# Performance work log

Hardware: AMD Instinct MI355X
Metric: run time of the kernel (lower is better)

The kernel has to match this reference:

```python
import jax, jax.numpy as jnp
import numpy as np

EPS = 1e-10

def setup_inputs() -> dict:
    key = jax.random.key(0)
    ks = jax.random.split(key, 7)
    B, S, C, H, W = 8, 4, 512, 64, 64
    Cq = C // 4
    x = jax.random.normal(ks[0], (B, S, C, H, W), dtype=jnp.float32)
    wq = jax.random.normal(ks[1], (S, Cq, C), dtype=jnp.float32) * 0.02
    bq = jax.random.normal(ks[2], (S, Cq), dtype=jnp.float32) * 0.02
    wk = jax.random.normal(ks[3], (S, Cq, C), dtype=jnp.float32) * 0.02
    bk = jax.random.normal(ks[4], (S, Cq), dtype=jnp.float32) * 0.02
    wv = jax.random.normal(ks[5], (S, C, C), dtype=jnp.float32) * 0.02
    bv = jax.random.normal(ks[6], (S, C), dtype=jnp.float32) * 0.02
    gamma = jnp.zeros((1,), dtype=jnp.float32)
    return {"x": x, "wq": wq, "bq": bq, "wk": wk, "bk": bk,
            "wv": wv, "bv": bv, "gamma": gamma}

def reference(x, wq, bq, wk, bk, wv, bv, gamma):
    # x: (B, S, C, H, W); per-scale 1x1 convs == per-pixel matmuls
    B, S, C, H, W = x.shape
    q = jnp.einsum('bschw,soc->bsohw', x, wq) + bq[None, :, :, None, None]
    k = jnp.einsum('bschw,soc->bsohw', x, wk) + bk[None, :, :, None, None]
    v = jnp.einsum('bschw,soc->bsohw', x, wv) + bv[None, :, :, None, None]
    pq = q.reshape(B, S, -1)                      # (B, S, D)
    pk = k.reshape(B, S, -1).transpose(0, 2, 1)   # (B, D, S)
    pv = v.reshape(B, S, -1)                      # (B, S, C*H*W)
    # L2 normalization (cosine similarity), matching torch eps placement
    A1 = pq / (jnp.sqrt(jnp.sum(pq * pq, axis=-1, keepdims=True)) + EPS)
    B1 = pk / (jnp.sqrt(jnp.sum(pk * pk, axis=1, keepdims=True)) + EPS)
    energy = jnp.einsum('bsd,bdt->bst', A1, B1)   # (B, S, S)
    attention = jax.nn.softmax(energy, axis=-1)
    out = jnp.einsum('bst,btd->bsd', attention, pv).reshape(B, S, C, H, W)
    out = gamma[0] * out + x
    # original returns list [out[:, i]] for i in range(S); return stacked tensor
    return out
```

## Files before the change

kernel.cpp:

```cpp
#include <hip/hip_runtime.h>
#include <hip/hip_bf16.h>

#define EPS_F 1e-10f

typedef short s16x8 __attribute__((ext_vector_type(8)));
typedef float f32x4 __attribute__((ext_vector_type(4)));
typedef unsigned short ushort_t;

constexpr int B_ = 8, S_ = 4, C_ = 512, Cq_ = 128, HW_ = 4096;
constexpr long long D_ = (long long)Cq_ * HW_;

__device__ inline float bf_lo(unsigned int u) { return __uint_as_float(u << 16); }
__device__ inline float bf_hi(unsigned int u) { return __uint_as_float(u & 0xffff0000u); }

__device__ inline ushort_t f2bf(float f) {
    __hip_bfloat16 h = __float2bfloat16(f);
    return *reinterpret_cast<ushort_t*>(&h);
}
__device__ inline unsigned int pack_bf2(float a, float b) {
    return (unsigned int)f2bf(a) | ((unsigned int)f2bf(b) << 16);
}

#define GLOAD16(gp, lp) __builtin_amdgcn_global_load_lds( \
    (const __attribute__((address_space(1))) unsigned int*)(gp), \
    (__attribute__((address_space(3))) unsigned int*)(lp), 16, 0, 0)

__global__ __launch_bounds__(256) void prep3(
    const float* __restrict__ wq, const float* __restrict__ wk,
    const float* __restrict__ wv,
    ushort_t* __restrict__ Wqk_pre, ushort_t* __restrict__ Wvb_pre,
    float* __restrict__ g4) {
    int gid = blockIdx.x * 256 + threadIdx.x;
    if (gid < 32 * 6 * 4) g4[gid] = 0.f;
    if (gid < 65536) {
        int s = gid >> 14;
        int kt = (gid >> 11) & 7;
        int row = (gid >> 3) & 255;
        int slot = gid & 7;
        int col = kt * 64 + ((slot ^ (row & 7)) << 3);
        const float* src = (row < 128)
            ? &wq[((size_t)s * 128 + row) * 512 + col]
            : &wk[((size_t)s * 128 + (row - 128)) * 512 + col];
        float4 f0 = *reinterpret_cast<const float4*>(src);
        float4 f1 = *reinterpret_cast<const float4*>(src + 4);
        uint4 o;
        o.x = pack_bf2(f0.x, f0.y); o.y = pack_bf2(f0.z, f0.w);
        o.z = pack_bf2(f1.x, f1.y); o.w = pack_bf2(f1.z, f1.w);
        *reinterpret_cast<uint4*>(Wqk_pre + (size_t)gid * 8) = o;
    } else {
        int c2 = gid - 65536;
        int t = c2 >> 15;
        int ct = (c2 >> 14) & 1;
        int kt = (c2 >> 11) & 7;
        int row = (c2 >> 3) & 255;
        int slot = c2 & 7;
        int col = kt * 64 + ((slot ^ (row & 7)) << 3);
        const float* src = &wv[((size_t)t * 512 + ct * 256 + row) * 512 + col];
        float4 f0 = *reinterpret_cast<const float4*>(src);
        float4 f1 = *reinterpret_cast<const float4*>(src + 4);
        uint4 o;
        o.x = pack_bf2(f0.x, f0.y); o.y = pack_bf2(f0.z, f0.w);
        o.z = pack_bf2(f1.x, f1.y); o.w = pack_bf2(f1.z, f1.w);
        *reinterpret_cast<uint4*>(Wvb_pre + (size_t)c2 * 8) = o;
    }
}

#define STAGE_A(tilebase, buf, Asarr)                                        \
    {                                                                        \
        const ushort_t* _tp = (tilebase);                                    \
        _Pragma("unroll")                                                    \
        for (int _i = 0; _i < 4; ++_i)                                       \
            GLOAD16(_tp + ((w4 + _i) << 9) + (lane << 3),                    \
                    &Asarr[buf][(w4 + _i) << 9]);                            \
    }

#define COMPUTE_STEP(buf, Asarr, Bsarr, accv)                                \
    {                                                                        \
        _Pragma("unroll")                                                    \
        for (int h = 0; h < 2; ++h) {                                        \
            s16x8 af0, af1, af2, af3, bf0, bf1;                              \
            af0 = *reinterpret_cast<const s16x8*>(                           \
                &Asarr[buf][(arow + 0 * 16 + li) * 64 + a_sl[h]]);           \
            af1 = *reinterpret_cast<const s16x8*>(                           \
                &Asarr[buf][(arow + 1 * 16 + li) * 64 + a_sl[h]]);           \
            af2 = *reinterpret_cast<const s16x8*>(                           \
                &Asarr[buf][(arow + 2 * 16 + li) * 64 + a_sl[h]]);           \
            af3 = *reinterpret_cast<const s16x8*>(                           \
                &Asarr[buf][(arow + 3 * 16 + li) * 64 + a_sl[h]]);           \
            bf0 = *reinterpret_cast<const s16x8*>(                           \
                &Bsarr[buf][bp0 * 64 + b_sl0[h]]);                           \
            bf1 = *reinterpret_cast<const s16x8*>(                           \
                &Bsarr[buf][bp1 * 64 + b_sl1[h]]);                           \
            accv[0][0] = __builtin_amdgcn_mfma_f32_16x16x32_bf16(af0, bf0, accv[0][0], 0, 0, 0); \
            accv[0][1] = __builtin_amdgcn_mfma_f32_16x16x32_bf16(af0, bf1, accv[0][1], 0, 0, 0); \
            accv[1][0] = __builtin_amdgcn_mfma_f32_16x16x32_bf16(af1, bf0, accv[1][0], 0, 0, 0); \
            accv[1][1] = __builtin_amdgcn_mfma_f32_16x16x32_bf16(af1, bf1, accv[1][1], 0, 0, 0); \
            accv[2][0] = __builtin_amdgcn_mfma_f32_16x16x32_bf16(af2, bf0, accv[2][0], 0, 0, 0); \
            accv[2][1] = __builtin_amdgcn_mfma_f32_16x16x32_bf16(af2, bf1, accv[2][1], 0, 0, 0); \
            accv[3][0] = __builtin_amdgcn_mfma_f32_16x16x32_bf16(af3, bf0, accv[3][0], 0, 0, 0); \
            accv[3][1] = __builtin_amdgcn_mfma_f32_16x16x32_bf16(af3, bf1, accv[3][1], 0, 0, 0); \
        }                                                                    \
    }

#define WRITE_B(buf, Bsarr, v0, v1)                                          \
    {                                                                        \
        float _vv[8] = {v0.x, v0.y, v0.z, v0.w, v1.x, v1.y, v1.z, v1.w};     \
        ushort_t* _d = &Bsarr[buf][bwbase];                                  \
        _Pragma("unroll")                                                    \
        for (int _j = 0; _j < 8; ++_j) _d[_j * 64] = f2bf(_vv[_j]);          \
    }

__global__ __launch_bounds__(512) void qk3(
    const ushort_t* __restrict__ Wqk_pre, const float* __restrict__ x,
    const float* __restrict__ bq, const float* __restrict__ bk,
    ushort_t* __restrict__ Qb, ushort_t* __restrict__ Kb) {

    const int bt = blockIdx.z;
    const int s = bt & 3;
    const int p0 = blockIdx.x * 64;

    __shared__ __align__(16) ushort_t As[2][16384];
    __shared__ __align__(16) ushort_t Bs[2][4096];

    const int tid = threadIdx.x;
    const int w = tid >> 6, lane = tid & 63;
    const int w4 = w * 4;
    const int wr = w >> 1, wc = w & 1;
    const int li = lane & 15, lk = lane >> 4;
    const int arow = wr * 64;
    int a_sl[2], b_sl0[2], b_sl1[2];
    const int bp0 = wc * 32 + 0 * 16 + li, bp1 = wc * 32 + 1 * 16 + li;
#pragma unroll
    for (int h = 0; h < 2; ++h) {
        a_sl[h] = (((h * 4 + lk) ^ (li & 7)) << 3);
        b_sl0[h] = (((h * 4 + lk) ^ ((bp0 >> 3) & 7)) << 3);
        b_sl1[h] = (((h * 4 + lk) ^ ((bp1 >> 3) & 7)) << 3);
    }
    const int sk = tid >> 3, sp = (tid & 7) * 8;
    const int bwbase = sp * 64 + (((sk >> 3) ^ (tid & 7)) << 3) + (sk & 7);

    const float* Bx = x + (size_t)bt * C_ * HW_ + p0 + sp;

    f32x4 acc[4][2];
#pragma unroll
    for (int mf = 0; mf < 4; ++mf)
#pragma unroll
        for (int nf = 0; nf < 2; ++nf) acc[mf][nf] = 0.f;

    STAGE_A(Wqk_pre + (((size_t)s * 8 + 0) << 14), 0, As);
    {
        const float* src = Bx + (size_t)sk * HW_;
        float4 v0 = *reinterpret_cast<const float4*>(src);
        float4 v1 = *reinterpret_cast<const float4*>(src + 4);
        WRITE_B(0, Bs, v0, v1);
    }
    __syncthreads();

    int cur = 0;
    for (int st = 0; st < 8; ++st) {
        float4 nb0, nb1;
        const bool more = (st < 7);
        if (more) {
            STAGE_A(Wqk_pre + (((size_t)s * 8 + st + 1) << 14), cur ^ 1, As);
            const float* src = Bx + (size_t)((st + 1) * 64 + sk) * HW_;
            nb0 = *reinterpret_cast<const float4*>(src);
            nb1 = *reinterpret_cast<const float4*>(src + 4);
        }
        COMPUTE_STEP(cur, As, Bs, acc);
        if (more) {
            WRITE_B(cur ^ 1, Bs, nb0, nb1);
            __syncthreads();
            cur ^= 1;
        }
    }

#pragma unroll
    for (int mf = 0; mf < 4; ++mf) {
#pragma unroll
        for (int r = 0; r < 4; ++r) {
            int m = wr * 64 + mf * 16 + lk * 4 + r;
            float bias = (m < 128) ? bq[s * 128 + m] : bk[s * 128 + (m - 128)];
#pragma unroll
            for (int nf = 0; nf < 2; ++nf) {
                int p = p0 + wc * 32 + nf * 16 + li;
                float vv = acc[mf][nf][r] + bias;
                if (m < 128)
                    Qb[(size_t)bt * D_ + (size_t)m * HW_ + p] = f2bf(vv);
                else
                    Kb[(size_t)bt * D_ + (size_t)(m - 128) * HW_ + p] = f2bf(vv);
            }
        }
    }
}

__global__ __launch_bounds__(256) void gram_part(
    const ushort_t* __restrict__ Q, const ushort_t* __restrict__ K,
    float* __restrict__ g4) {

    const int u = blockIdx.x, ch = blockIdx.y, bs = blockIdx.z;
    const int b = bs >> 2;
    const ushort_t *pa, *pb;
    if (u < 4)       { pa = Q + (size_t)bs * D_; pb = K + (size_t)(b * 4 + u) * D_; }
    else if (u == 4) { pa = pb = Q + (size_t)bs * D_; }
    else             { pa = pb = K + (size_t)bs * D_; }

    const size_t off = (size_t)ch * (D_ / 4);
    const uint4* va = reinterpret_cast<const uint4*>(pa + off);
    const uint4* vb = reinterpret_cast<const uint4*>(pb + off);
    const int n8 = (int)(D_ / 4 / 8);

    float acc = 0.f;
    for (int i = threadIdx.x; i < n8; i += 256) {
        uint4 a = va[i], c = vb[i];
        acc += bf_lo(a.x) * bf_lo(c.x) + bf_hi(a.x) * bf_hi(c.x);
        acc += bf_lo(a.y) * bf_lo(c.y) + bf_hi(a.y) * bf_hi(c.y);
        acc += bf_lo(a.z) * bf_lo(c.z) + bf_hi(a.z) * bf_hi(c.z);
        acc += bf_lo(a.w) * bf_lo(c.w) + bf_hi(a.w) * bf_hi(c.w);
    }
#pragma unroll
    for (int o = 32; o > 0; o >>= 1) acc += __shfl_down(acc, o);

    __shared__ float wsum[4];
    const int lane = threadIdx.x & 63, wid = threadIdx.x >> 6;
    if (lane == 0) wsum[wid] = acc;
    __syncthreads();
    if (threadIdx.x == 0)
        g4[(size_t)(bs * 6 + u) * 4 + ch] = wsum[0] + wsum[1] + wsum[2] + wsum[3];
}

__global__ void att_k(const float* __restrict__ g4, float* __restrict__ att) {
    const int b = threadIdx.x;
    if (b >= B_) return;
    auto g = [&](int s, int u) {
        const float* p = g4 + (size_t)((b * 4 + s) * 6 + u) * 4;
        return p[0] + p[1] + p[2] + p[3];
    };
    float nq[4], nk[4];
#pragma unroll
    for (int s = 0; s < 4; ++s) {
        nq[s] = sqrtf(g(s, 4)) + EPS_F;
        nk[s] = sqrtf(g(s, 5)) + EPS_F;
    }
#pragma unroll
    for (int s = 0; s < 4; ++s) {
        float e[4], m = -1e30f;
#pragma unroll
        for (int t = 0; t < 4; ++t) {
            e[t] = g(s, t) / (nq[s] * nk[t]);
            m = fmaxf(m, e[t]);
        }
        float sum = 0.f;
#pragma unroll
        for (int t = 0; t < 4; ++t) { e[t] = expf(e[t] - m); sum += e[t]; }
#pragma unroll
        for (int t = 0; t < 4; ++t) att[(size_t)(b * 4 + s) * 4 + t] = e[t] / sum;
    }
}

__global__ __launch_bounds__(512) void vblend3(
    const ushort_t* __restrict__ Wvb_pre, const float* __restrict__ x,
    const float* __restrict__ bv, const float* __restrict__ att,
    const float* __restrict__ gamma, float* __restrict__ out) {

    const int b = blockIdx.z;
    const int ct = blockIdx.y;
    const int p0 = blockIdx.x * 64;

    __shared__ __align__(16) ushort_t As[2][16384];
    __shared__ __align__(16) ushort_t Bs[2][4096];

    const int tid = threadIdx.x;
    const int w = tid >> 6, lane = tid & 63;
    const int w4 = w * 4;
    const int wr = w >> 1, wc = w & 1;
    const int li = lane & 15, lk = lane >> 4;
    const int arow = wr * 64;
    int a_sl[2], b_sl0[2], b_sl1[2];
    const int bp0 = wc * 32 + 0 * 16 + li, bp1 = wc * 32 + 1 * 16 + li;
#pragma unroll
    for (int h = 0; h < 2; ++h) {
        a_sl[h] = (((h * 4 + lk) ^ (li & 7)) << 3);
        b_sl0[h] = (((h * 4 + lk) ^ ((bp0 >> 3) & 7)) << 3);
        b_sl1[h] = (((h * 4 + lk) ^ ((bp1 >> 3) & 7)) << 3);
    }
    const int sk = tid >> 3, sp = (tid & 7) * 8;
    const int bwbase = sp * 64 + (((sk >> 3) ^ (tid & 7)) << 3) + (sk & 7);
    const float gm = gamma[0];

    f32x4 mst[4][4][2];
#pragma unroll
    for (int so = 0; so < 4; ++so)
#pragma unroll
        for (int mf = 0; mf < 4; ++mf)
#pragma unroll
            for (int nf = 0; nf < 2; ++nf) mst[so][mf][nf] = 0.f;

    f32x4 acc[4][2];
#pragma unroll
    for (int mf = 0; mf < 4; ++mf)
#pragma unroll
        for (int nf = 0; nf < 2; ++nf) acc[mf][nf] = 0.f;

    STAGE_A(Wvb_pre + (((size_t)(0 * 2 + ct) * 8 + 0) << 14), 0, As);
    {
        const float* src = x + ((size_t)(b * 4 + 0) * 512 + sk) * HW_ + p0 + sp;
        float4 v0 = *reinterpret_cast<const float4*>(src);
        float4 v1 = *reinterpret_cast<const float4*>(src + 4);
        WRITE_B(0, Bs, v0, v1);
    }
    __syncthreads();

    int cur = 0;
    for (int st = 0; st < 32; ++st) {
        float4 nb0, nb1;
        const bool more = (st < 31);
        if (more) {
            const int t2 = (st + 1) >> 3, kt2 = (st + 1) & 7;
            STAGE_A(Wvb_pre + (((size_t)(t2 * 2 + ct) * 8 + kt2) << 14), cur ^ 1, As);
            const float* src =
                x + ((size_t)(b * 4 + t2) * 512 + kt2 * 64 + sk) * HW_ + p0 + sp;
            nb0 = *reinterpret_cast<const float4*>(src);
            nb1 = *reinterpret_cast<const float4*>(src + 4);
        }
        COMPUTE_STEP(cur, As, Bs, acc);
        if ((st & 7) == 7) {
            const int t = st >> 3;
#pragma unroll
            for (int so = 0; so < 4; ++so) {
                const float wt = att[(size_t)(b * 4 + so) * 4 + t];
#pragma unroll
                for (int mf = 0; mf < 4; ++mf)
#pragma unroll
                    for (int nf = 0; nf < 2; ++nf)
                        mst[so][mf][nf] += wt * acc[mf][nf];
            }
#pragma unroll
            for (int mf = 0; mf < 4; ++mf)
#pragma unroll
                for (int nf = 0; nf < 2; ++nf) acc[mf][nf] = 0.f;
        }
        if (more) {
            WRITE_B(cur ^ 1, Bs, nb0, nb1);
            __syncthreads();
            cur ^= 1;
        }
    }

    const int c0 = ct * 256;
#pragma unroll
    for (int mf = 0; mf < 4; ++mf) {
#pragma unroll
        for (int r = 0; r < 4; ++r) {
            int c = c0 + wr * 64 + mf * 16 + lk * 4 + r;
            float bvv[4];
#pragma unroll
            for (int t = 0; t < 4; ++t) bvv[t] = bv[(size_t)t * 512 + c];
#pragma unroll
            for (int so = 0; so < 4; ++so) {
                float a0 = att[(size_t)(b * 4 + so) * 4 + 0];
                float a1 = att[(size_t)(b * 4 + so) * 4 + 1];
                float a2 = att[(size_t)(b * 4 + so) * 4 + 2];
                float a3 = att[(size_t)(b * 4 + so) * 4 + 3];
                float bsum = a0 * bvv[0] + a1 * bvv[1] + a2 * bvv[2] + a3 * bvv[3];
#pragma unroll
                for (int nf = 0; nf < 2; ++nf) {
                    int p = p0 + wc * 32 + nf * 16 + li;
                    size_t off = ((size_t)(b * 4 + so) * C_ + c) * HW_ + p;
                    out[off] = gm * (mst[so][mf][nf][r] + bsum) + x[off];
                }
            }
        }
    }
}

extern "C" void kernel_launch(void* const* d_in, const int* in_sizes, int n_in,
                              void* d_out, int out_size, void* d_ws, size_t ws_size,
                              hipStream_t stream) {
    const float* x     = (const float*)d_in[0];
    const float* wq    = (const float*)d_in[1];
    const float* bq    = (const float*)d_in[2];
    const float* wk    = (const float*)d_in[3];
    const float* bk    = (const float*)d_in[4];
    const float* wv    = (const float*)d_in[5];
    const float* bv    = (const float*)d_in[6];
    const float* gamma = (const float*)d_in[7];
    float* out = (float*)d_out;

    char* ws = (char*)d_ws;
    const size_t qk_elems = (size_t)B_ * S_ * Cq_ * HW_;
    ushort_t* Qb      = (ushort_t*)ws;
    ushort_t* Kb      = Qb + qk_elems;
    ushort_t* Wqk_pre = Kb + qk_elems;
    ushort_t* Wvb_pre = Wqk_pre + (size_t)4 * 8 * 256 * 64;
    float*    g4      = (float*)(Wvb_pre + (size_t)4 * 2 * 8 * 256 * 64);
    float*    att     = g4 + 32 * 6 * 4;

    prep3<<<768, 256, 0, stream>>>(wq, wk, wv, Wqk_pre, Wvb_pre, g4);
    qk3<<<dim3(64, 1, 32), 512, 0, stream>>>(Wqk_pre, x, bq, bk, Qb, Kb);
    gram_part<<<dim3(6, 4, 32), 256, 0, stream>>>(Qb, Kb, g4);
    att_k<<<1, 64, 0, stream>>>(g4, att);
    vblend3<<<dim3(64, 2, 8), 512, 0, stream>>>(Wvb_pre, x, bv, att, gamma, out);
}
```

Baseline: 414.0 us.

## Triple-buffer GEMM pipelines, remap blocks, and fuse gram reductions per batch

The QK and V-blend GEMM kernels move from a double-buffered loop with __syncthreads to a shared triple-buffered pipeline. It uses explicit vmcnt/lgkmcnt waits, raw s_barrier, MFMA priority boosting, and a new XOR swizzle for B-tile writes. Blocks are launched on a 1D grid with an id remap that interleaves the ordering, likely for L2/XCD locality. The gram kernel now reads each Q/K chunk once and accumulates all 24 dot products per batch instead of launching separate blocks per pair, and attention weights are cached in LDS. The larger LDS footprint from triple buffering may reduce occupancy.

```diff
diff --git a/kernel.cpp b/kernel.cpp
--- a/kernel.cpp
+++ b/kernel.cpp
@@ -20,10 +20,20 @@
 __device__ inline unsigned int pack_bf2(float a, float b) {
     return (unsigned int)f2bf(a) | ((unsigned int)f2bf(b) << 16);
 }
+__device__ inline float dot8(uint4 a, uint4 b) {
+    return bf_lo(a.x) * bf_lo(b.x) + bf_hi(a.x) * bf_hi(b.x)
+         + bf_lo(a.y) * bf_lo(b.y) + bf_hi(a.y) * bf_hi(b.y)
+         + bf_lo(a.z) * bf_lo(b.z) + bf_hi(a.z) * bf_hi(b.z)
+         + bf_lo(a.w) * bf_lo(b.w) + bf_hi(a.w) * bf_hi(b.w);
+}
 
 #define GLOAD16(gp, lp) __builtin_amdgcn_global_load_lds( \
     (const __attribute__((address_space(1))) unsigned int*)(gp), \
     (__attribute__((address_space(3))) unsigned int*)(lp), 16, 0, 0)
+
+#define VMCNT(n) asm volatile("s_waitcnt vmcnt(" #n ")" ::: "memory")
+#define LGK0     asm volatile("s_waitcnt lgkmcnt(0)" ::: "memory")
+#define MFMA16(a, b, c) __builtin_amdgcn_mfma_f32_16x16x32_bf16(a, b, c, 0, 0, 0)
 
 __global__ __launch_bounds__(256) void prep3(
     const float* __restrict__ wq, const float* __restrict__ wk,
@@ -31,7 +41,7 @@
     ushort_t* __restrict__ Wqk_pre, ushort_t* __restrict__ Wvb_pre,
     float* __restrict__ g4) {
     int gid = blockIdx.x * 256 + threadIdx.x;
-    if (gid < 32 * 6 * 4) g4[gid] = 0.f;
+    if (gid < 8 * 24 * 16) g4[gid] = 0.f;
     if (gid < 65536) {
         int s = gid >> 14;
         int kt = (gid >> 11) & 7;
@@ -65,113 +75,130 @@
     }
 }
 
-#define STAGE_A(tilebase, buf, Asarr)                                        \
+#define STAGE_A(T, bufidx)                                                   \
+    { const ushort_t* _tp = ASRC(T);                                         \
+      ushort_t* _ld = &AsAll[(bufidx) * 16384];                              \
+      _Pragma("unroll")                                                      \
+      for (int _i = 0; _i < 4; ++_i)                                         \
+          GLOAD16(_tp + ((w4 + _i) << 9) + (lane << 3),                      \
+                  _ld + ((w4 + _i) << 9)); }
+
+#define LOAD_B(T, V0, V1)                                                    \
+    { const float* _s = BSRC(T);                                             \
+      V0 = *reinterpret_cast<const float4*>(_s);                             \
+      V1 = *reinterpret_cast<const float4*>(_s + 4); }
+
+#define WRITE_B(bufidx, V0, V1)                                              \
+    { float _vv[8] = {V0.x, V0.y, V0.z, V0.w, V1.x, V1.y, V1.z, V1.w};       \
+      ushort_t* _bd = &BsAll[(bufidx) * 4096 + bw_row0];                     \
+      _Pragma("unroll")                                                      \
+      for (int _j = 0; _j < 8; ++_j)                                         \
+          _bd[_j * 64 + ((bw_sb ^ _j) << 3)] = f2bf(_vv[_j]); }
+
+#define COMPUTE(bufidx)                                                      \
+    { const int _ab = (bufidx) * 16384, _bb = (bufidx) * 4096;               \
+      _Pragma("unroll")                                                      \
+      for (int h = 0; h < 2; ++h) {                                          \
+          s16x8 af0 = *reinterpret_cast<const s16x8*>(                       \
+              &AsAll[_ab + (arow + 0 * 16 + li) * 64 + a_sl[h]]);            \
+          s16x8 af1 = *reinterpret_cast<const s16x8*>(                       \
+              &AsAll[_ab + (arow + 1 * 16 + li) * 64 + a_sl[h]]);            \
+          s16x8 af2 = *reinterpret_cast<const s16x8*>(                       \
+              &AsAll[_ab + (arow + 2 * 16 + li) * 64 + a_sl[h]]);            \
+          s16x8 af3 = *reinterpret_cast<const s16x8*>(                       \
+              &AsAll[_ab + (arow + 3 * 16 + li) * 64 + a_sl[h]]);            \
+          s16x8 bf0 = *reinterpret_cast<const s16x8*>(                       \
+              &BsAll[_bb + bp0 * 64 + b_sl0[h]]);                            \
+          s16x8 bf1 = *reinterpret_cast<const s16x8*>(                       \
+              &BsAll[_bb + bp1 * 64 + b_sl1[h]]);                            \
+          __builtin_amdgcn_s_setprio(1);                                     \
+          acc[0][0] = MFMA16(af0, bf0, acc[0][0]);                           \
+          acc[0][1] = MFMA16(af0, bf1, acc[0][1]);                           \
+          acc[1][0] = MFMA16(af1, bf0, acc[1][0]);                           \
+          acc[1][1] = MFMA16(af1, bf1, acc[1][1]);                           \
+          acc[2][0] = MFMA16(af2, bf0, acc[2][0]);                           \
+          acc[2][1] = MFMA16(af2, bf1, acc[2][1]);                           \
+          acc[3][0] = MFMA16(af3, bf0, acc[3][0]);                           \
+          acc[3][1] = MFMA16(af3, bf1, acc[3][1]);                           \
+          __builtin_amdgcn_s_setprio(0);                                     \
+      } }
+
+#define PIPE_PROLOGUE()                                                      \
+    LOAD_B(0, nbE0, nbE1);                                                   \
+    STAGE_A(0, 0);                                                           \
+    LOAD_B(1, nbO0, nbO1);                                                   \
+    STAGE_A(1, 1);                                                           \
+    VMCNT(10);                                                               \
+    WRITE_B(0, nbE0, nbE1);                                                  \
+    VMCNT(6);                                                                \
+    LGK0;                                                                    \
+    __builtin_amdgcn_s_barrier();
+
+#define PIPE_ITER(T, WB0, WB1, LB0, LB1)                                     \
     {                                                                        \
-        const ushort_t* _tp = (tilebase);                                    \
+        const int _t = (T);                                                  \
+        if (_t + 1 < NT) { VMCNT(4); WRITE_B(oN, WB0, WB1); }                \
+        if (_t + 2 < NT) { LOAD_B(_t + 2, LB0, LB1); STAGE_A(_t + 2, oNN); } \
+        COMPUTE(oC);                                                         \
+        ITER_EXTRA(_t);                                                      \
+        if (_t + 1 < NT) {                                                   \
+            if (_t + 2 < NT) { VMCNT(6); } else { VMCNT(0); }                \
+            LGK0;                                                            \
+            __builtin_amdgcn_s_barrier();                                    \
+        }                                                                    \
+        int _r = oC; oC = oN; oN = oNN; oNN = _r;                            \
+    }
+
+#define PIPE_COMMON_DECLS()                                                  \
+    const int tid = threadIdx.x;                                             \
+    const int w = tid >> 6, lane = tid & 63;                                 \
+    const int w4 = w * 4;                                                    \
+    const int wr = w >> 1, wc = w & 1;                                       \
+    const int li = lane & 15, lk = lane >> 4;                                \
+    const int arow = wr * 64;                                                \
+    const int bp0 = wc * 32 + li, bp1 = wc * 32 + 16 + li;                   \
+    int a_sl[2], b_sl0[2], b_sl1[2];                                         \
+    _Pragma("unroll")                                                        \
+    for (int h = 0; h < 2; ++h) {                                            \
+        a_sl[h] = (((h * 4 + lk) ^ (li & 7)) << 3);                          \
+        b_sl0[h] = (((h * 4 + lk) ^ ((bp0 >> 3) & 7) ^ (bp0 & 7)) << 3);     \
+        b_sl1[h] = (((h * 4 + lk) ^ ((bp1 >> 3) & 7) ^ (bp1 & 7)) << 3);     \
+    }                                                                        \
+    const int sk = tid >> 3, sp = (tid & 7) * 8;                             \
+    const int bw_row0 = sp * 64 + ((tid >> 3) & 7);                          \
+    const int bw_sb = (tid >> 6) ^ (tid & 7);                                \
+    int oC = 0, oN = 1, oNN = 2;                                             \
+    float4 nbE0, nbE1, nbO0, nbO1;                                           \
+    f32x4 acc[4][2];                                                         \
+    _Pragma("unroll")                                                        \
+    for (int mf = 0; mf < 4; ++mf)                                           \
         _Pragma("unroll")                                                    \
-        for (int _i = 0; _i < 4; ++_i)                                       \
-            GLOAD16(_tp + ((w4 + _i) << 9) + (lane << 3),                    \
-                    &Asarr[buf][(w4 + _i) << 9]);                            \
-    }
-
-#define COMPUTE_STEP(buf, Asarr, Bsarr, accv)                                \
-    {                                                                        \
-        _Pragma("unroll")                                                    \
-        for (int h = 0; h < 2; ++h) {                                        \
-            s16x8 af0, af1, af2, af3, bf0, bf1;                              \
-            af0 = *reinterpret_cast<const s16x8*>(                           \
-                &Asarr[buf][(arow + 0 * 16 + li) * 64 + a_sl[h]]);           \
-            af1 = *reinterpret_cast<const s16x8*>(                           \
-                &Asarr[buf][(arow + 1 * 16 + li) * 64 + a_sl[h]]);           \
-            af2 = *reinterpret_cast<const s16x8*>(                           \
-                &Asarr[buf][(arow + 2 * 16 + li) * 64 + a_sl[h]]);           \
-            af3 = *reinterpret_cast<const s16x8*>(                           \
-                &Asarr[buf][(arow + 3 * 16 + li) * 64 + a_sl[h]]);           \
-            bf0 = *reinterpret_cast<const s16x8*>(                           \
-                &Bsarr[buf][bp0 * 64 + b_sl0[h]]);                           \
-            bf1 = *reinterpret_cast<const s16x8*>(                           \
-                &Bsarr[buf][bp1 * 64 + b_sl1[h]]);                           \
-            accv[0][0] = __builtin_amdgcn_mfma_f32_16x16x32_bf16(af0, bf0, accv[0][0], 0, 0, 0); \
-            accv[0][1] = __builtin_amdgcn_mfma_f32_16x16x32_bf16(af0, bf1, accv[0][1], 0, 0, 0); \
-            accv[1][0] = __builtin_amdgcn_mfma_f32_16x16x32_bf16(af1, bf0, accv[1][0], 0, 0, 0); \
-            accv[1][1] = __builtin_amdgcn_mfma_f32_16x16x32_bf16(af1, bf1, accv[1][1], 0, 0, 0); \
-            accv[2][0] = __builtin_amdgcn_mfma_f32_16x16x32_bf16(af2, bf0, accv[2][0], 0, 0, 0); \
-            accv[2][1] = __builtin_amdgcn_mfma_f32_16x16x32_bf16(af2, bf1, accv[2][1], 0, 0, 0); \
-            accv[3][0] = __builtin_amdgcn_mfma_f32_16x16x32_bf16(af3, bf0, accv[3][0], 0, 0, 0); \
-            accv[3][1] = __builtin_amdgcn_mfma_f32_16x16x32_bf16(af3, bf1, accv[3][1], 0, 0, 0); \
-        }                                                                    \
-    }
-
-#define WRITE_B(buf, Bsarr, v0, v1)                                          \
-    {                                                                        \
-        float _vv[8] = {v0.x, v0.y, v0.z, v0.w, v1.x, v1.y, v1.z, v1.w};     \
-        ushort_t* _d = &Bsarr[buf][bwbase];                                  \
-        _Pragma("unroll")                                                    \
-        for (int _j = 0; _j < 8; ++_j) _d[_j * 64] = f2bf(_vv[_j]);          \
-    }
-
-__global__ __launch_bounds__(512) void qk3(
+        for (int nf = 0; nf < 2; ++nf) acc[mf][nf] = 0.f;
+
+#define ASRC(T) (Wqk_pre + ((size_t)(s * 8 + (T)) << 14))
+#define BSRC(T) (x + (size_t)bt * C_ * HW_ + (size_t)((T) * 64 + sk) * HW_ + p0 + sp)
+#define ITER_EXTRA(T)
+
+__global__ __launch_bounds__(512) void qk4(
     const ushort_t* __restrict__ Wqk_pre, const float* __restrict__ x,
     const float* __restrict__ bq, const float* __restrict__ bk,
     ushort_t* __restrict__ Qb, ushort_t* __restrict__ Kb) {
 
-    const int bt = blockIdx.z;
+    constexpr int NT = 8;
+    const int id = ((blockIdx.x & 7) << 8) | (blockIdx.x >> 3);
+    const int bt = id >> 6;
     const int s = bt & 3;
-    const int p0 = blockIdx.x * 64;
-
-    __shared__ __align__(16) ushort_t As[2][16384];
-    __shared__ __align__(16) ushort_t Bs[2][4096];
-
-    const int tid = threadIdx.x;
-    const int w = tid >> 6, lane = tid & 63;
-    const int w4 = w * 4;
-    const int wr = w >> 1, wc = w & 1;
-    const int li = lane & 15, lk = lane >> 4;
-    const int arow = wr * 64;
-    int a_sl[2], b_sl0[2], b_sl1[2];
-    const int bp0 = wc * 32 + 0 * 16 + li, bp1 = wc * 32 + 1 * 16 + li;
-#pragma unroll
-    for (int h = 0; h < 2; ++h) {
-        a_sl[h] = (((h * 4 + lk) ^ (li & 7)) << 3);
-        b_sl0[h] = (((h * 4 + lk) ^ ((bp0 >> 3) & 7)) << 3);
-        b_sl1[h] = (((h * 4 + lk) ^ ((bp1 >> 3) & 7)) << 3);
-    }
-    const int sk = tid >> 3, sp = (tid & 7) * 8;
-    const int bwbase = sp * 64 + (((sk >> 3) ^ (tid & 7)) << 3) + (sk & 7);
-
-    const float* Bx = x + (size_t)bt * C_ * HW_ + p0 + sp;
-
-    f32x4 acc[4][2];
-#pragma unroll
-    for (int mf = 0; mf < 4; ++mf)
-#pragma unroll
-        for (int nf = 0; nf < 2; ++nf) acc[mf][nf] = 0.f;
-
-    STAGE_A(Wqk_pre + (((size_t)s * 8 + 0) << 14), 0, As);
-    {
-        const float* src = Bx + (size_t)sk * HW_;
-        float4 v0 = *reinterpret_cast<const float4*>(src);
-        float4 v1 = *reinterpret_cast<const float4*>(src + 4);
-        WRITE_B(0, Bs, v0, v1);
-    }
-    __syncthreads();
-
-    int cur = 0;
-    for (int st = 0; st < 8; ++st) {
-        float4 nb0, nb1;
-        const bool more = (st < 7);
-        if (more) {
-            STAGE_A(Wqk_pre + (((size_t)s * 8 + st + 1) << 14), cur ^ 1, As);
-            const float* src = Bx + (size_t)((st + 1) * 64 + sk) * HW_;
-            nb0 = *reinterpret_cast<const float4*>(src);
-            nb1 = *reinterpret_cast<const float4*>(src + 4);
-        }
-        COMPUTE_STEP(cur, As, Bs, acc);
-        if (more) {
-            WRITE_B(cur ^ 1, Bs, nb0, nb1);
-            __syncthreads();
-            cur ^= 1;
-        }
+    const int p0 = (id & 63) * 64;
+
+    __shared__ __align__(16) ushort_t AsAll[3 * 16384];
+    __shared__ __align__(16) ushort_t BsAll[3 * 4096];
+
+    PIPE_COMMON_DECLS();
+    PIPE_PROLOGUE();
+
+    for (int t0 = 0; t0 < NT; t0 += 2) {
+        PIPE_ITER(t0,     nbO0, nbO1, nbE0, nbE1);
+        PIPE_ITER(t0 + 1, nbE0, nbE1, nbO0, nbO1);
     }
 
 #pragma unroll
@@ -192,160 +219,67 @@
         }
     }
 }
-
-__global__ __launch_bounds__(256) void gram_part(
-    const ushort_t* __restrict__ Q, const ushort_t* __restrict__ K,
-    float* __restrict__ g4) {
-
-    const int u = blockIdx.x, ch = blockIdx.y, bs = blockIdx.z;
-    const int b = bs >> 2;
-    const ushort_t *pa, *pb;
-    if (u < 4)       { pa = Q + (size_t)bs * D_; pb = K + (size_t)(b * 4 + u) * D_; }
-    else if (u == 4) { pa = pb = Q + (size_t)bs * D_; }
-    else             { pa = pb = K + (size_t)bs * D_; }
-
-    const size_t off = (size_t)ch * (D_ / 4);
-    const uint4* va = reinterpret_cast<const uint4*>(pa + off);
-    const uint4* vb = reinterpret_cast<const uint4*>(pb + off);
-    const int n8 = (int)(D_ / 4 / 8);
-
-    float acc = 0.f;
-    for (int i = threadIdx.x; i < n8; i += 256) {
-        uint4 a = va[i], c = vb[i];
-        acc += bf_lo(a.x) * bf_lo(c.x) + bf_hi(a.x) * bf_hi(c.x);
-        acc += bf_lo(a.y) * bf_lo(c.y) + bf_hi(a.y) * bf_hi(c.y);
-        acc += bf_lo(a.z) * bf_lo(c.z) + bf_hi(a.z) * bf_hi(c.z);
-        acc += bf_lo(a.w) * bf_lo(c.w) + bf_hi(a.w) * bf_hi(c.w);
-    }
-#pragma unroll
-    for (int o = 32; o > 0; o >>= 1) acc += __shfl_down(acc, o);
-
-    __shared__ float wsum[4];
-    const int lane = threadIdx.x & 63, wid = threadIdx.x >> 6;
-    if (lane == 0) wsum[wid] = acc;
-    __syncthreads();
-    if (threadIdx.x == 0)
-        g4[(size_t)(bs * 6 + u) * 4 + ch] = wsum[0] + wsum[1] + wsum[2] + wsum[3];
-}
-
-__global__ void att_k(const float* __restrict__ g4, float* __restrict__ att) {
-    const int b = threadIdx.x;
-    if (b >= B_) return;
-    auto g = [&](int s, int u) {
-        const float* p = g4 + (size_t)((b * 4 + s) * 6 + u) * 4;
-        return p[0] + p[1] + p[2] + p[3];
-    };
-    float nq[4], nk[4];
-#pragma unroll
-    for (int s = 0; s < 4; ++s) {
-        nq[s] = sqrtf(g(s, 4)) + EPS_F;
-        nk[s] = sqrtf(g(s, 5)) + EPS_F;
-    }
-#pragma unroll
-    for (int s = 0; s < 4; ++s) {
-        float e[4], m = -1e30f;
-#pragma unroll
-        for (int t = 0; t < 4; ++t) {
-            e[t] = g(s, t) / (nq[s] * nk[t]);
-            m = fmaxf(m, e[t]);
-        }
-        float sum = 0.f;
-#pragma unroll
-        for (int t = 0; t < 4; ++t) { e[t] = expf(e[t] - m); sum += e[t]; }
-#pragma unroll
-        for (int t = 0; t < 4; ++t) att[(size_t)(b * 4 + s) * 4 + t] = e[t] / sum;
-    }
-}
-
-__global__ __launch_bounds__(512) void vblend3(
+#undef ASRC
+#undef BSRC
+#undef ITER_EXTRA
+
+#define ASRC(T) (Wvb_pre + (((size_t)(((T) >> 3) * 2 + ct) * 8 + ((T) & 7)) << 14))
+#define BSRC(T) (x + ((size_t)(b * 4 + ((T) >> 3)) * 512 + ((T) & 7) * 64 + sk) * HW_ + p0 + sp)
+#define ITER_EXTRA(T)                                                        \
+    if (((T) & 7) == 7) {                                                    \
+        const int _t2 = (T) >> 3;                                            \
+        float _wv[4];                                                        \
+        _Pragma("unroll")                                                    \
+        for (int _so = 0; _so < 4; ++_so) _wv[_so] = attL[_so * 4 + _t2];    \
+        _Pragma("unroll")                                                    \
+        for (int _so = 0; _so < 4; ++_so)                                    \
+            _Pragma("unroll")                                                \
+            for (int _mf = 0; _mf < 4; ++_mf)                                \
+                _Pragma("unroll")                                            \
+                for (int _nf = 0; _nf < 2; ++_nf)                            \
+                    mst[_so][_mf][_nf] += _wv[_so] * acc[_mf][_nf];          \
+        _Pragma("unroll")                                                    \
+        for (int _mf = 0; _mf < 4; ++_mf)                                    \
+            _Pragma("unroll")                                                \
+            for (int _nf = 0; _nf < 2; ++_nf) acc[_mf][_nf] = 0.f;           \
+    }
+
+__global__ __launch_bounds__(512) void vblend4(
     const ushort_t* __restrict__ Wvb_pre, const float* __restrict__ x,
     const float* __restrict__ bv, const float* __restrict__ att,
     const float* __restrict__ gamma, float* __restrict__ out) {
 
-    const int b = blockIdx.z;
-    const int ct = blockIdx.y;
-    const int p0 = blockIdx.x * 64;
-
-    __shared__ __align__(16) ushort_t As[2][16384];
-    __shared__ __align__(16) ushort_t Bs[2][4096];
-
-    const int tid = threadIdx.x;
-    const int w = tid >> 6, lane = tid & 63;
-    const int w4 = w * 4;
-    const int wr = w >> 1, wc = w & 1;
-    const int li = lane & 15, lk = lane >> 4;
-    const int arow = wr * 64;
-    int a_sl[2], b_sl0[2], b_sl1[2];
-    const int bp0 = wc * 32 + 0 * 16 + li, bp1 = wc * 32 + 1 * 16 + li;
-#pragma unroll
-    for (int h = 0; h < 2; ++h) {
-        a_sl[h] = (((h * 4 + lk) ^ (li & 7)) << 3);
-        b_sl0[h] = (((h * 4 + lk) ^ ((bp0 >> 3) & 7)) << 3);
-        b_sl1[h] = (((h * 4 + lk) ^ ((bp1 >> 3) & 7)) << 3);
-    }
-    const int sk = tid >> 3, sp = (tid & 7) * 8;
-    const int bwbase = sp * 64 + (((sk >> 3) ^ (tid & 7)) << 3) + (sk & 7);
+    constexpr int NT = 32;
+    const int id = ((blockIdx.x & 7) << 7) | (blockIdx.x >> 3);
+    const int b = id >> 7;
+    const int ct = (id >> 6) & 1;
+    const int p0 = (id & 63) * 64;
+
+    __shared__ __align__(16) ushort_t AsAll[3 * 16384];
+    __shared__ __align__(16) ushort_t BsAll[3 * 4096];
+    __shared__ float attL[16];
+
+    if (threadIdx.x < 16) attL[threadIdx.x] = att[b * 16 + threadIdx.x];
+    __syncthreads();
+
+    PIPE_COMMON_DECLS();
+
+    f32x4 mst[4][4][2];
+#pragma unroll
+    for (int so = 0; so < 4; ++so)
+#pragma unroll
+        for (int mf = 0; mf < 4; ++mf)
+#pragma unroll
+            for (int nf = 0; nf < 2; ++nf) mst[so][mf][nf] = 0.f;
+
+    PIPE_PROLOGUE();
+
+    for (int t0 = 0; t0 < NT; t0 += 2) {
+        PIPE_ITER(t0,     nbO0, nbO1, nbE0, nbE1);
+        PIPE_ITER(t0 + 1, nbE0, nbE1, nbO0, nbO1);
+    }
+
     const float gm = gamma[0];
-
-    f32x4 mst[4][4][2];
-#pragma unroll
-    for (int so = 0; so < 4; ++so)
-#pragma unroll
-        for (int mf = 0; mf < 4; ++mf)
-#pragma unroll
-            for (int nf = 0; nf < 2; ++nf) mst[so][mf][nf] = 0.f;
-
-    f32x4 acc[4][2];
-#pragma unroll
-    for (int mf = 0; mf < 4; ++mf)
-#pragma unroll
-        for (int nf = 0; nf < 2; ++nf) acc[mf][nf] = 0.f;
-
-    STAGE_A(Wvb_pre + (((size_t)(0 * 2 + ct) * 8 + 0) << 14), 0, As);
-    {
-        const float* src = x + ((size_t)(b * 4 + 0) * 512 + sk) * HW_ + p0 + sp;
-        float4 v0 = *reinterpret_cast<const float4*>(src);
-        float4 v1 = *reinterpret_cast<const float4*>(src + 4);
-        WRITE_B(0, Bs, v0, v1);
-    }
-    __syncthreads();
-
-    int cur = 0;
-    for (int st = 0; st < 32; ++st) {
-        float4 nb0, nb1;
-        const bool more = (st < 31);
-        if (more) {
-            const int t2 = (st + 1) >> 3, kt2 = (st + 1) & 7;
-            STAGE_A(Wvb_pre + (((size_t)(t2 * 2 + ct) * 8 + kt2) << 14), cur ^ 1, As);
-            const float* src =
-                x + ((size_t)(b * 4 + t2) * 512 + kt2 * 64 + sk) * HW_ + p0 + sp;
-            nb0 = *reinterpret_cast<const float4*>(src);
-            nb1 = *reinterpret_cast<const float4*>(src + 4);
-        }
-        COMPUTE_STEP(cur, As, Bs, acc);
-        if ((st & 7) == 7) {
-            const int t = st >> 3;
-#pragma unroll
-            for (int so = 0; so < 4; ++so) {
-                const float wt = att[(size_t)(b * 4 + so) * 4 + t];
-#pragma unroll
-                for (int mf = 0; mf < 4; ++mf)
-#pragma unroll
-                    for (int nf = 0; nf < 2; ++nf)
-                        mst[so][mf][nf] += wt * acc[mf][nf];
-            }
-#pragma unroll
-            for (int mf = 0; mf < 4; ++mf)
-#pragma unroll
-                for (int nf = 0; nf < 2; ++nf) acc[mf][nf] = 0.f;
-        }
-        if (more) {
-            WRITE_B(cur ^ 1, Bs, nb0, nb1);
-            __syncthreads();
-            cur ^= 1;
-        }
-    }
-
     const int c0 = ct * 256;
 #pragma unroll
     for (int mf = 0; mf < 4; ++mf) {
@@ -357,11 +291,8 @@
             for (int t = 0; t < 4; ++t) bvv[t] = bv[(size_t)t * 512 + c];
 #pragma unroll
             for (int so = 0; so < 4; ++so) {
-                float a0 = att[(size_t)(b * 4 + so) * 4 + 0];
-                float a1 = att[(size_t)(b * 4 + so) * 4 + 1];
-                float a2 = att[(size_t)(b * 4 + so) * 4 + 2];
-                float a3 = att[(size_t)(b * 4 + so) * 4 + 3];
-                float bsum = a0 * bvv[0] + a1 * bvv[1] + a2 * bvv[2] + a3 * bvv[3];
+                float bsum = attL[so * 4 + 0] * bvv[0] + attL[so * 4 + 1] * bvv[1]
+                           + attL[so * 4 + 2] * bvv[2] + attL[so * 4 + 3] * bvv[3];
 #pragma unroll
                 for (int nf = 0; nf < 2; ++nf) {
                     int p = p0 + wc * 32 + nf * 16 + li;
@@ -370,6 +301,94 @@
                 }
             }
         }
+    }
+}
+#undef ASRC
+#undef BSRC
+#undef ITER_EXTRA
+
+__global__ __launch_bounds__(256) void gram5(
+    const ushort_t* __restrict__ Q, const ushort_t* __restrict__ K,
+    float* __restrict__ g4) {
+
+    const int ch = blockIdx.x;
+    const int b  = blockIdx.y;
+    const size_t base = (size_t)ch * (D_ / 16);
+
+    const uint4* qv[4];
+    const uint4* kv[4];
+#pragma unroll
+    for (int s = 0; s < 4; ++s) {
+        qv[s] = reinterpret_cast<const uint4*>(Q + (size_t)(b * 4 + s) * D_ + base);
+        kv[s] = reinterpret_cast<const uint4*>(K + (size_t)(b * 4 + s) * D_ + base);
+    }
+
+    float accr[24];
+#pragma unroll
+    for (int e = 0; e < 24; ++e) accr[e] = 0.f;
+
+    const int n8 = (int)(D_ / 16 / 8);
+    for (int i = threadIdx.x; i < n8; i += 256) {
+        uint4 qa[4], ka[4];
+#pragma unroll
+        for (int s = 0; s < 4; ++s) { qa[s] = qv[s][i]; ka[s] = kv[s][i]; }
+#pragma unroll
+        for (int s = 0; s < 4; ++s) {
+#pragma unroll
+            for (int u = 0; u < 4; ++u) accr[s * 4 + u] += dot8(qa[s], ka[u]);
+            accr[16 + s] += dot8(qa[s], qa[s]);
+            accr[20 + s] += dot8(ka[s], ka[s]);
+        }
+    }
+
+    __shared__ float red[4][24];
+    const int lane = threadIdx.x & 63, wid = threadIdx.x >> 6;
+#pragma unroll
+    for (int e = 0; e < 24; ++e) {
+        float v = accr[e];
+#pragma unroll
+        for (int o = 32; o > 0; o >>= 1) v += __shfl_down(v, o);
+        if (lane == 0) red[wid][e] = v;
+    }
+    __syncthreads();
+    if (threadIdx.x < 24) {
+        float t = red[0][threadIdx.x] + red[1][threadIdx.x]
+                + red[2][threadIdx.x] + red[3][threadIdx.x];
+        g4[((size_t)b * 24 + threadIdx.x) * 16 + ch] = t;
+    }
+}
+
+__global__ void att_k5(const float* __restrict__ g4, float* __restrict__ att) {
+    const int b = threadIdx.x;
+    if (b >= B_) return;
+    float e_[24];
+#pragma unroll
+    for (int e = 0; e < 24; ++e) {
+        const float* p = g4 + ((size_t)b * 24 + e) * 16;
+        float t = 0.f;
+#pragma unroll
+        for (int ch = 0; ch < 16; ++ch) t += p[ch];
+        e_[e] = t;
+    }
+    float nq[4], nk[4];
+#pragma unroll
+    for (int s = 0; s < 4; ++s) {
+        nq[s] = sqrtf(e_[16 + s]) + EPS_F;
+        nk[s] = sqrtf(e_[20 + s]) + EPS_F;
+    }
+#pragma unroll
+    for (int s = 0; s < 4; ++s) {
+        float e[4], m = -1e30f;
+#pragma unroll
+        for (int t = 0; t < 4; ++t) {
+            e[t] = e_[s * 4 + t] / (nq[s] * nk[t]);
+            m = fmaxf(m, e[t]);
+        }
+        float sum = 0.f;
+#pragma unroll
+        for (int t = 0; t < 4; ++t) { e[t] = expf(e[t] - m); sum += e[t]; }
+#pragma unroll
+        for (int t = 0; t < 4; ++t) att[(size_t)(b * 4 + s) * 4 + t] = e[t] / sum;
     }
 }
 
@@ -393,11 +412,11 @@
     ushort_t* Wqk_pre = Kb + qk_elems;
     ushort_t* Wvb_pre = Wqk_pre + (size_t)4 * 8 * 256 * 64;
     float*    g4      = (float*)(Wvb_pre + (size_t)4 * 2 * 8 * 256 * 64);
-    float*    att     = g4 + 32 * 6 * 4;
+    float*    att     = g4 + 8 * 24 * 16;
 
     prep3<<<768, 256, 0, stream>>>(wq, wk, wv, Wqk_pre, Wvb_pre, g4);
-    qk3<<<dim3(64, 1, 32), 512, 0, stream>>>(Wqk_pre, x, bq, bk, Qb, Kb);
-    gram_part<<<dim3(6, 4, 32), 256, 0, stream>>>(Qb, Kb, g4);
-    att_k<<<1, 64, 0, stream>>>(g4, att);
-    vblend3<<<dim3(64, 2, 8), 512, 0, stream>>>(Wvb_pre, x, bv, att, gamma, out);
-}
+    qk4<<<2048, 512, 0, stream>>>(Wqk_pre, x, bq, bk, Qb, Kb);
+    gram5<<<dim3(16, 8), 256, 0, stream>>>(Qb, Kb, g4);
+    att_k5<<<1, 64, 0, stream>>>(g4, att);
+    vblend4<<<1024, 512, 0, stream>>>(Wvb_pre, x, bv, att, gamma, out);
+}
```

Measured after the change: 429.7 us. 1.04x slower.
